# Optimization experiments

Measured on AMD Instinct MI355X. Metric: run time of the kernel, lower is better.

## Reference

```python
import jax, jax.numpy as jnp
import numpy as np

N = 50000      # nodes
E = 600000     # edges (avg degree 12)
F_IN = 64      # raw node features
HID = 128      # hidden_size
HEADS = 8
DH = HID // HEADS  # 16, per-head dim = out_channels
C = 10         # classes
L = 3          # num_gnn_layers


def setup_inputs() -> dict:
    key = jax.random.key(0)
    ks = jax.random.split(key, 12)
    g = lambda k, shape, fan: jax.random.normal(k, shape, jnp.float32) / np.float32(np.sqrt(fan))
    return {
        "x": jax.random.normal(ks[0], (N, F_IN), jnp.float32),
        "edge_index": jax.random.randint(ks[1], (2, E), 0, N, dtype=jnp.int32),
        "distance": jax.random.uniform(ks[2], (E, 1), jnp.float32),
        "Wq": g(ks[3], (L, HID, HID), HID), "bq": jnp.zeros((L, HID), jnp.float32),
        "Wk": g(ks[4], (L, HID, HID), HID), "bk": jnp.zeros((L, HID), jnp.float32),
        "Wv": g(ks[5], (L, HID, HID), HID), "bv": jnp.zeros((L, HID), jnp.float32),
        "We": g(ks[6], (L, 1, HID), 1),
        "Ws": g(ks[7], (L, HID, HID), HID), "bs": jnp.zeros((L, HID), jnp.float32),
        "ln_g": jnp.ones((L, HID), jnp.float32), "ln_b": jnp.zeros((L, HID), jnp.float32),
        "W_before": g(ks[8], (F_IN, HID), F_IN), "b_before": jnp.zeros((HID,), jnp.float32),
        "W_after": g(ks[9], (HID, C), HID), "b_after": jnp.zeros((C,), jnp.float32),
    }


def _layer_norm(h, gamma, beta):
    m = h.mean(-1, keepdims=True)
    v = ((h - m) ** 2).mean(-1, keepdims=True)
    return (h - m) * jax.lax.rsqrt(v + 1e-5) * gamma + beta


def _transformer_conv(h, src, dst, ea, Wq, bq, Wk, bk, Wv, bv, We, Ws, bs):
    # PyG TransformerConv (concat=True, beta=False, root_weight=True), eval mode (no dropout)
    q = (h @ Wq + bq).reshape(-1, HEADS, DH)   # [N,H,D]
    k = (h @ Wk + bk).reshape(-1, HEADS, DH)
    v = (h @ Wv + bv).reshape(-1, HEADS, DH)
    e = (ea @ We).reshape(-1, HEADS, DH)       # [E,H,D] edge embedding (no bias)
    ke = k[src] + e                            # gather keys along edges
    alpha = (q[dst] * ke).sum(-1) / np.float32(np.sqrt(DH))  # [E,H]
    # segment softmax over incoming edges per destination node
    amax = jax.ops.segment_max(alpha, dst, num_segments=N)
    amax = jnp.where(jnp.isfinite(amax), amax, 0.0)
    ex = jnp.exp(alpha - amax[dst])
    den = jax.ops.segment_sum(ex, dst, num_segments=N)
    a = ex / (den[dst] + 1e-16)                # [E,H]
    msg = (v[src] + e) * a[..., None]          # weighted values
    out = jax.ops.segment_sum(msg, dst, num_segments=N).reshape(-1, HEADS * DH)
    return out + h @ Ws + bs                   # root/skip connection


def reference(x, edge_index, distance, Wq, bq, Wk, bk, Wv, bv, We, Ws, bs,
              ln_g, ln_b, W_before, b_before, W_after, b_after):
    src, dst = edge_index[0], edge_index[1]
    h = jax.nn.relu(x @ W_before + b_before)   # fcnn_before
    for i in range(L):
        h = _transformer_conv(h, src, dst, distance,
                              Wq[i], bq[i], Wk[i], bk[i], Wv[i], bv[i],
                              We[i], Ws[i], bs[i])
        if i < L - 1:
            h = jax.nn.relu(_layer_norm(h, ln_g[i], ln_b[i]))
    # fcnn_after
    h = jax.nn.relu(_layer_norm(h, ln_g[L - 1], ln_b[L - 1]))
    h = h @ W_after + b_after
    return jax.nn.log_softmax(h, axis=1)
```

## Files before the change

kernel.cpp:

```cpp
#include <hip/hip_runtime.h>
#include <cstdint>
#include <cstddef>

#define NN 50000
#define NE 600000
#define FIN 64
#define HID 128
#define NCLS 10
#define NLAYER 3

#define QSCALE 0.36067376022224085f

typedef __bf16 bf16x8 __attribute__((ext_vector_type(8)));
typedef float f32x4 __attribute__((ext_vector_type(4)));
typedef float f32x2 __attribute__((ext_vector_type(2)));

__device__ __forceinline__ unsigned short f2bf(float f) {
    unsigned int u = __builtin_bit_cast(unsigned int, f);
    u += 0x7fffu + ((u >> 16) & 1u);
    return (unsigned short)(u >> 16);
}
__device__ __forceinline__ float bf2f(unsigned short s) {
    unsigned int u = ((unsigned int)s) << 16;
    return __builtin_bit_cast(float, u);
}
__device__ __forceinline__ float lo16f(unsigned int w) {
    return __builtin_bit_cast(float, w << 16);
}
__device__ __forceinline__ float hi16f(unsigned int w) {
    return __builtin_bit_cast(float, w & 0xffff0000u);
}

__global__ __launch_bounds__(256) void k_count(const int* __restrict__ edst,
                                               int* __restrict__ counts) {
    int e = blockIdx.x * 256 + threadIdx.x;
    if (e < NE) atomicAdd(&counts[edst[e]], 1);
}

__global__ __launch_bounds__(512) void k_scan1(const int* __restrict__ counts,
                                               int* __restrict__ row_ptr,
                                               int* __restrict__ partials, int n) {
    __shared__ int sm[512];
    int tid = threadIdx.x;
    int i = blockIdx.x * 512 + tid;
    int v = (i < n) ? counts[i] : 0;
    sm[tid] = v;
    __syncthreads();
    #pragma unroll
    for (int off = 1; off < 512; off <<= 1) {
        int t = (tid >= off) ? sm[tid - off] : 0;
        __syncthreads();
        sm[tid] += t;
        __syncthreads();
    }
    if (i < n) row_ptr[i] = sm[tid] - v;
    if (tid == 511) partials[blockIdx.x] = sm[511];
}

__global__ __launch_bounds__(128) void k_scan2(int* __restrict__ partials, int nb) {
    __shared__ int sm[128];
    int t = threadIdx.x;
    int v = (t < nb) ? partials[t] : 0;
    sm[t] = v;
    __syncthreads();
    #pragma unroll
    for (int off = 1; off < 128; off <<= 1) {
        int x = (t >= off) ? sm[t - off] : 0;
        __syncthreads();
        sm[t] += x;
        __syncthreads();
    }
    if (t < nb) partials[t] = sm[t] - v;
}

__global__ __launch_bounds__(512) void k_scan3(int* __restrict__ row_ptr,
                                               const int* __restrict__ partials, int n) {
    int i = blockIdx.x * 512 + threadIdx.x;
    if (i < n) row_ptr[i] += partials[blockIdx.x];
}

__global__ __launch_bounds__(256) void k_fill(const int* __restrict__ esrc,
                                              const int* __restrict__ edst,
                                              const float* __restrict__ dist,
                                              int* __restrict__ cursor,
                                              const int* __restrict__ row_ptr,
                                              int2* __restrict__ srcd) {
    int e = blockIdx.x * 256 + threadIdx.x;
    if (e < NE) {
        int d = edst[e];
        int pos = atomicAdd(&cursor[d], 1);
        srcd[row_ptr[d] + pos] = make_int2(esrc[e], __float_as_int(dist[e]));
    }
}

__global__ __launch_bounds__(256) void k_wprep(
    const float* __restrict__ Wq, const float* __restrict__ Wk,
    const float* __restrict__ Wv, const float* __restrict__ Ws,
    const float* __restrict__ Wbe, const float* __restrict__ Waf,
    unsigned short* __restrict__ Wt12,
    unsigned short* __restrict__ Wbt,
    float* __restrict__ Wat)
{
    int blk = blockIdx.x;
    int tid = threadIdx.x;
    if (blk < 768) {
        int m = blk >> 6;
        int l = m >> 2, which = m & 3;
        const float* src;
        if (which == 0) src = Wq; else if (which == 1) src = Wk;
        else if (which == 2) src = Wv; else src = Ws;
        src += (size_t)l * HID * HID;
        int idx = (blk & 63) * 256 + tid;
        int c = idx >> 7, k = idx & 127;
        Wt12[(size_t)m * 16384 + (size_t)c * 128 + k] = f2bf(src[(size_t)k * 128 + c]);
    } else if (blk < 800) {
        int idx = (blk - 768) * 256 + tid;
        int c = idx >> 6, k = idx & 63;
        Wbt[(size_t)c * 64 + k] = f2bf(Wbe[(size_t)k * 128 + c]);
    } else {
        int i = (blk - 800) * 256 + tid;
        if (i < 1280) {
            int c = i >> 7, f = i & 127;
            Wat[i] = Waf[f * 10 + c];
        }
    }
}

__global__ __launch_bounds__(512) void k_qkvs(
    const unsigned short* __restrict__ Ab, int nrows,
    const unsigned short* __restrict__ Wt,
    const float* __restrict__ bq, const float* __restrict__ bk,
    const float* __restrict__ bv, const float* __restrict__ bs,
    unsigned short* __restrict__ qb,
    unsigned char* __restrict__ kv8,
    unsigned short* __restrict__ hsb)
{
    const int tid = threadIdx.x;
    const int w = tid >> 6, lane = tid & 63;
    const int m = w >> 1, ch = w & 1;
    const float* bias = (m == 0) ? bq : (m == 1) ? bk : (m == 2) ? bv : bs;
    const unsigned short* Wm = Wt + (size_t)m * 16384;
    const int lc = lane & 15, lk = lane >> 4;

    bf16x8 b[4][4];
    float bb[4];
    #pragma unroll
    for (int ct = 0; ct < 4; ++ct) {
        int col = ch * 64 + ct * 16 + lc;
        bb[ct] = bias[col];
        #pragma unroll
        for (int kb = 0; kb < 4; ++kb)
            b[ct][kb] = *(const bf16x8*)(Wm + (size_t)col * 128 + kb * 32 + lk * 8);
    }

    const int r0 = blockIdx.x * 64;
    #pragma unroll
    for (int rt = 0; rt < 4; ++rt) {
        const int arow = r0 + rt * 16 + lc;
        bf16x8 z = {};
        bf16x8 a[4];
        #pragma unroll
        for (int kb = 0; kb < 4; ++kb)
            a[kb] = (arow < nrows) ? *(const bf16x8*)(Ab + (size_t)arow * 128 + kb * 32 + lk * 8) : z;
        #pragma unroll
        for (int ct = 0; ct < 4; ++ct) {
            f32x4 acc = {0.f, 0.f, 0.f, 0.f};
            #pragma unroll
            for (int kb = 0; kb < 4; ++kb)
                acc = __builtin_amdgcn_mfma_f32_16x16x32_bf16(a[kb], b[ct][kb], acc, 0, 0, 0);
            const int col = ch * 64 + ct * 16 + lc;
            #pragma unroll
            for (int i = 0; i < 4; ++i) {
                int r = r0 + rt * 16 + lk * 4 + i;
                if (r >= nrows) continue;
                float val = acc[i] + bb[ct];
                if (m == 0) {
                    qb[(size_t)r * 128 + col] = f2bf(val * QSCALE);
                } else if (m == 1) {
                    unsigned int pk = __builtin_amdgcn_cvt_pk_fp8_f32(val, val, 0, false);
                    kv8[(size_t)r * 256 + col] = (unsigned char)(pk & 0xff);
                } else if (m == 2) {
                    unsigned int pk = __builtin_amdgcn_cvt_pk_fp8_f32(val, val, 0, false);
                    kv8[(size_t)r * 256 + 128 + col] = (unsigned char)(pk & 0xff);
                } else {
                    hsb[(size_t)r * 128 + col] = f2bf(val);
                }
            }
        }
    }
}

__global__ __launch_bounds__(256) void k_gin(
    const float* __restrict__ x, int nrows,
    const unsigned short* __restrict__ Wt,
    const float* __restrict__ bias,
    unsigned short* __restrict__ hb)
{
    const int tid = threadIdx.x;
    const int w = tid >> 6, lane = tid & 63;
    const int row0 = blockIdx.x * 64 + w * 16;
    const int lc = lane & 15, lk = lane >> 4;
    const int arow = row0 + lc;
    const bool rv = arow < nrows;

    bf16x8 a[2];
    #pragma unroll
    for (int kb = 0; kb < 2; ++kb) {
        union { bf16x8 v; unsigned short u[8]; } t;
        #pragma unroll
        for (int q = 0; q < 2; ++q) {
            float4 f = rv ? *(const float4*)(x + (size_t)arow * 64 + kb * 32 + lk * 8 + q * 4)
                          : make_float4(0.f, 0.f, 0.f, 0.f);
            t.u[q * 4 + 0] = f2bf(f.x); t.u[q * 4 + 1] = f2bf(f.y);
            t.u[q * 4 + 2] = f2bf(f.z); t.u[q * 4 + 3] = f2bf(f.w);
        }
        a[kb] = t.v;
    }

    const int cbase = lk * 4;
    #pragma unroll
    for (int ct = 0; ct < 8; ++ct) {
        const int bcol = ct * 16 + lc;
        f32x4 acc = {0.f, 0.f, 0.f, 0.f};
        #pragma unroll
        for (int kb = 0; kb < 2; ++kb) {
            bf16x8 b = *(const bf16x8*)(Wt + (size_t)bcol * 64 + kb * 32 + lk * 8);
            acc = __builtin_amdgcn_mfma_f32_16x16x32_bf16(a[kb], b, acc, 0, 0, 0);
        }
        const float bv_ = bias[bcol];
        #pragma unroll
        for (int i = 0; i < 4; ++i) {
            int r = row0 + cbase + i;
            if (r >= nrows) continue;
            hb[(size_t)r * 128 + bcol] = f2bf(fmaxf(acc[i] + bv_, 0.f));
        }
    }
}

#define LOADB(bi, kw, vw, dd, vv) {                                       \
    int rel_ = (bi) * 8 + j;                                              \
    vv = rel_ < cnt;                                                      \
    if (vv) {                                                             \
        int2 e2_ = srcd[beg + rel_];                                      \
        dd = __int_as_float(e2_.y);                                       \
        const unsigned char* kr_ = kvb + (size_t)e2_.x * 256 + h * 16;    \
        *(uint4*)(kw) = *(const uint4*)(kr_);                             \
        *(uint4*)(vw) = *(const uint4*)(kr_ + 128);                       \
    } else {                                                              \
        dd = 0.f;                                                         \
        _Pragma("unroll")                                                 \
        for (int z_ = 0; z_ < 4; ++z_) { (kw)[z_] = 0u; (vw)[z_] = 0u; }  \
    } }

#define COMPB(kw, vw, dd, vv) {                                           \
    float p_ = 0.f;                                                       \
    _Pragma("unroll")                                                     \
    for (int w4 = 0; w4 < 4; ++w4) {                                      \
        f32x2 k01_ = __builtin_amdgcn_cvt_pk_f32_fp8((kw)[w4], false);    \
        f32x2 k23_ = __builtin_amdgcn_cvt_pk_f32_fp8((kw)[w4], true);     \
        p_ = fmaf(qf[4 * w4 + 0], k01_.x, p_);                            \
        p_ = fmaf(qf[4 * w4 + 1], k01_.y, p_);                            \
        p_ = fmaf(qf[4 * w4 + 2], k23_.x, p_);                            \
        p_ = fmaf(qf[4 * w4 + 3], k23_.y, p_);                            \
    }                                                                     \
    p_ = fmaf(dd, qwe, p_);                                               \
    float wgt_ = (vv) ? exp2f(p_) : 0.f;                                  \
    s += wgt_;                                                            \
    sd = fmaf(dd, wgt_, sd);                                              \
    _Pragma("unroll")                                                     \
    for (int w4 = 0; w4 < 4; ++w4) {                                      \
        f32x2 v01_ = __builtin_amdgcn_cvt_pk_f32_fp8((vw)[w4], false);    \
        f32x2 v23_ = __builtin_amdgcn_cvt_pk_f32_fp8((vw)[w4], true);     \
        vacc[4 * w4 + 0] = fmaf(v01_.x, wgt_, vacc[4 * w4 + 0]);          \
        vacc[4 * w4 + 1] = fmaf(v01_.y, wgt_, vacc[4 * w4 + 1]);          \
        vacc[4 * w4 + 2] = fmaf(v23_.x, wgt_, vacc[4 * w4 + 2]);          \
        vacc[4 * w4 + 3] = fmaf(v23_.y, wgt_, vacc[4 * w4 + 3]);          \
    } }

template <int LAST>
__global__ __launch_bounds__(256) void k_attn(
    const unsigned short* __restrict__ qb,
    const unsigned short* __restrict__ hsb,
    const unsigned char* __restrict__ kvb,
    const int2* __restrict__ srcd,
    const float* __restrict__ We,
    const int* __restrict__ row_ptr,
    const float* __restrict__ lng,
    const float* __restrict__ lnb,
    unsigned short* __restrict__ hb,
    const float* __restrict__ Wat,
    const float* __restrict__ ba,
    float* __restrict__ out, int nnodes)
{
    const int wid = threadIdx.x >> 6;
    const int lane = threadIdx.x & 63;
    const int n = blockIdx.x * 4 + wid;
    if (n >= nnodes) return;
    const int h = lane >> 3, j = lane & 7;
    const int c0 = lane * 2;

    unsigned int uq[8];
    *(uint4*)(uq)     = *(const uint4*)(qb + (size_t)n * 128 + h * 16);
    *(uint4*)(uq + 4) = *(const uint4*)(qb + (size_t)n * 128 + h * 16 + 8);
    float qf[16];
    #pragma unroll
    for (int d = 0; d < 8; ++d) {
        qf[2 * d]     = lo16f(uq[d]);
        qf[2 * d + 1] = hi16f(uq[d]);
    }
    float qwe = 0.f;
    #pragma unroll
    for (int d4 = 0; d4 < 4; ++d4) {
        float4 wv = *(const float4*)(We + h * 16 + d4 * 4);
        qwe = fmaf(qf[d4 * 4 + 0], wv.x, qwe);
        qwe = fmaf(qf[d4 * 4 + 1], wv.y, qwe);
        qwe = fmaf(qf[d4 * 4 + 2], wv.z, qwe);
        qwe = fmaf(qf[d4 * 4 + 3], wv.w, qwe);
    }

    const int beg = row_ptr[n];
    const int cnt = row_ptr[n + 1] - beg;
    float s = 0.f, sd = 0.f;
    float vacc[16];
    #pragma unroll
    for (int d = 0; d < 16; ++d) vacc[d] = 0.f;

    if (cnt > 0) {
        const int nbatch = (cnt + 7) >> 3;
        unsigned int kwA[4], vwA[4], kwB[4], vwB[4], kwC[4], vwC[4];
        float dA = 0.f, dB = 0.f, dC = 0.f;
        bool vA = false, vB = false, vC = false;
        LOADB(0, kwA, vwA, dA, vA);
        if (1 < nbatch) LOADB(1, kwB, vwB, dB, vB);
        int b = 0;
        while (true) {
            if (b + 2 < nbatch) LOADB(b + 2, kwC, vwC, dC, vC);
            COMPB(kwA, vwA, dA, vA);
            if (++b >= nbatch) break;
            if (b + 2 < nbatch) LOADB(b + 2, kwA, vwA, dA, vA);
            COMPB(kwB, vwB, dB, vB);
            if (++b >= nbatch) break;
            if (b + 2 < nbatch) LOADB(b + 2, kwB, vwB, dB, vB);
            COMPB(kwC, vwC, dC, vC);
            if (++b >= nbatch) break;
        }
    }

    #pragma unroll
    for (int msk = 1; msk < 8; msk <<= 1) {
        s  += __shfl_xor(s, msk);
        sd += __shfl_xor(sd, msk);
    }
    const bool b4 = (lane & 4) != 0;
    float c8[8];
    #pragma unroll
    for (int i = 0; i < 8; ++i) {
        float sendv = b4 ? vacc[i] : vacc[8 + i];
        float keep  = b4 ? vacc[8 + i] : vacc[i];
        c8[i] = keep + __shfl_xor(sendv, 4);
    }
    const bool b2 = (lane & 2) != 0;
    float c4[4];
    #pragma unroll
    for (int i = 0; i < 4; ++i) {
        float sendv = b2 ? c8[i] : c8[4 + i];
        float keep  = b2 ? c8[4 + i] : c8[i];
        c4[i] = keep + __shfl_xor(sendv, 2);
    }
    const bool b1 = (lane & 1) != 0;
    float c2[2];
    #pragma unroll
    for (int i = 0; i < 2; ++i) {
        float sendv = b1 ? c4[i] : c4[2 + i];
        float keep  = b1 ? c4[2 + i] : c4[i];
        c2[i] = keep + __shfl_xor(sendv, 1);
    }

    const float inv = 1.f / (s + 1e-16f);
    const float we0 = We[c0], we1 = We[c0 + 1];
    const ushort2 hu = *(const ushort2*)(hsb + (size_t)n * 128 + c0);
    float o0 = fmaf(fmaf(we0, sd, c2[0]), inv, bf2f(hu.x));
    float o1 = fmaf(fmaf(we1, sd, c2[1]), inv, bf2f(hu.y));

    float t = o0 + o1;
    #pragma unroll
    for (int off = 1; off < 64; off <<= 1) t += __shfl_xor(t, off);
    float mean = t * 0.0078125f;
    float d0 = o0 - mean, d1 = o1 - mean;
    float vv2 = d0 * d0 + d1 * d1;
    #pragma unroll
    for (int off = 1; off < 64; off <<= 1) vv2 += __shfl_xor(vv2, off);
    float rstd = rsqrtf(vv2 * 0.0078125f + 1e-5f);
    float y0 = fmaxf(d0 * rstd * lng[c0] + lnb[c0], 0.f);
    float y1 = fmaxf(d1 * rstd * lng[c0 + 1] + lnb[c0 + 1], 0.f);

    if (LAST) {
        float lg[NCLS];
        #pragma unroll
        for (int c = 0; c < NCLS; ++c) {
            float2 wv = *(const float2*)(Wat + c * 128 + c0);
            float p = fmaf(y0, wv.x, y1 * wv.y);
            #pragma unroll
            for (int msk = 1; msk < 64; msk <<= 1) p += __shfl_xor(p, msk);
            lg[c] = p + ba[c];
        }
        float mx = lg[0];
        #pragma unroll
        for (int c = 1; c < NCLS; ++c) mx = fmaxf(mx, lg[c]);
        float sum = 0.f;
        #pragma unroll
        for (int c = 0; c < NCLS; ++c) sum += __expf(lg[c] - mx);
        float lse = mx + __logf(sum);
        if (lane == 0) {
            #pragma unroll
            for (int c = 0; c < NCLS; ++c) out[(size_t)n * NCLS + c] = lg[c] - lse;
        }
    } else {
        ushort2 o;
        o.x = f2bf(y0);
        o.y = f2bf(y1);
        *(ushort2*)(hb + (size_t)n * 128 + c0) = o;
    }
}

extern "C" void kernel_launch(void* const* d_in, const int* in_sizes, int n_in,
                              void* d_out, int out_size, void* d_ws, size_t ws_size,
                              hipStream_t stream)
{
    const float* x    = (const float*)d_in[0];
    const int*   ei   = (const int*)d_in[1];
    const float* dist = (const float*)d_in[2];
    const float* Wq   = (const float*)d_in[3];
    const float* bq   = (const float*)d_in[4];
    const float* Wk   = (const float*)d_in[5];
    const float* bk   = (const float*)d_in[6];
    const float* Wv   = (const float*)d_in[7];
    const float* bv   = (const float*)d_in[8];
    const float* We   = (const float*)d_in[9];
    const float* Wsk  = (const float*)d_in[10];
    const float* bs   = (const float*)d_in[11];
    const float* lng  = (const float*)d_in[12];
    const float* lnb  = (const float*)d_in[13];
    const float* Wbe  = (const float*)d_in[14];
    const float* bbe  = (const float*)d_in[15];
    const float* Waf  = (const float*)d_in[16];
    const float* baf  = (const float*)d_in[17];
    float* out = (float*)d_out;
    const int* esrc = ei;
    const int* edst = ei + NE;

    char* ws = (char*)d_ws;
    size_t off = 0;
    unsigned short* qb  = (unsigned short*)(ws + off); off += 12800000;
    unsigned short* hsb = (unsigned short*)(ws + off); off += 12800000;
    unsigned char*  kv8 = (unsigned char*)(ws + off);  off += 12800000;
    unsigned short* hb  = (unsigned short*)(ws + off); off += 12800000;
    unsigned short* Wt12 = (unsigned short*)(ws + off); off += 393216;
    unsigned short* Wbt  = (unsigned short*)(ws + off); off += 16384;
    float* Wat = (float*)(ws + off);   off += 5120;
    int* counts   = (int*)(ws + off);  off += 200192;
    int* cursor   = (int*)(ws + off);  off += 200192;
    int* row_ptr  = (int*)(ws + off);  off += 200192;
    int* partials = (int*)(ws + off);  off += 512;
    int2* srcd    = (int2*)(ws + off); off += (size_t)NE * 8;

    hipMemsetAsync(counts, 0, (NN + 1) * sizeof(int), stream);
    hipMemsetAsync(cursor, 0, NN * sizeof(int), stream);
    k_count<<<(NE + 255) / 256, 256, 0, stream>>>(edst, counts);
    int nsb = (NN + 1 + 511) / 512;
    k_scan1<<<nsb, 512, 0, stream>>>(counts, row_ptr, partials, NN + 1);
    k_scan2<<<1, 128, 0, stream>>>(partials, nsb);
    k_scan3<<<nsb, 512, 0, stream>>>(row_ptr, partials, NN + 1);
    k_fill<<<(NE + 255) / 256, 256, 0, stream>>>(esrc, edst, dist, cursor, row_ptr, srcd);

    k_wprep<<<805, 256, 0, stream>>>(Wq, Wk, Wv, Wsk, Wbe, Waf, Wt12, Wbt, Wat);

    const int ngb = (NN + 63) / 64;

    k_gin<<<ngb, 256, 0, stream>>>(x, NN, Wbt, bbe, hb);

    for (int l = 0; l < NLAYER; ++l) {
        const unsigned short* wt = Wt12 + (size_t)l * 4 * 16384;
        k_qkvs<<<ngb, 512, 0, stream>>>(hb, NN, wt,
            bq + l * HID, bk + l * HID, bv + l * HID, bs + l * HID,
            qb, kv8, hsb);
        if (l < NLAYER - 1) {
            k_attn<0><<<(NN + 3) / 4, 256, 0, stream>>>(qb, hsb, kv8, srcd, We + l * HID,
                row_ptr, lng + l * HID, lnb + l * HID, hb, nullptr, nullptr, nullptr, NN);
        } else {
            k_attn<1><<<(NN + 3) / 4, 256, 0, stream>>>(qb, hsb, kv8, srcd, We + l * HID,
                row_ptr, lng + l * HID, lnb + l * HID, hb, Wat, baf, out, NN);
        }
    }
}
```

Measured before the change: 396.1 us.

## Process two nodes per wave in attention, vectorize GEMM stores, fuse prep kernels

```diff
diff --git a/kernel.cpp b/kernel.cpp
--- a/kernel.cpp
+++ b/kernel.cpp
@@ -31,75 +31,14 @@
     return __builtin_bit_cast(float, w & 0xffff0000u);
 }
 
-__global__ __launch_bounds__(256) void k_count(const int* __restrict__ edst,
-                                               int* __restrict__ counts) {
-    int e = blockIdx.x * 256 + threadIdx.x;
-    if (e < NE) atomicAdd(&counts[edst[e]], 1);
-}
-
-__global__ __launch_bounds__(512) void k_scan1(const int* __restrict__ counts,
-                                               int* __restrict__ row_ptr,
-                                               int* __restrict__ partials, int n) {
-    __shared__ int sm[512];
-    int tid = threadIdx.x;
-    int i = blockIdx.x * 512 + tid;
-    int v = (i < n) ? counts[i] : 0;
-    sm[tid] = v;
-    __syncthreads();
-    #pragma unroll
-    for (int off = 1; off < 512; off <<= 1) {
-        int t = (tid >= off) ? sm[tid - off] : 0;
-        __syncthreads();
-        sm[tid] += t;
-        __syncthreads();
-    }
-    if (i < n) row_ptr[i] = sm[tid] - v;
-    if (tid == 511) partials[blockIdx.x] = sm[511];
-}
-
-__global__ __launch_bounds__(128) void k_scan2(int* __restrict__ partials, int nb) {
-    __shared__ int sm[128];
-    int t = threadIdx.x;
-    int v = (t < nb) ? partials[t] : 0;
-    sm[t] = v;
-    __syncthreads();
-    #pragma unroll
-    for (int off = 1; off < 128; off <<= 1) {
-        int x = (t >= off) ? sm[t - off] : 0;
-        __syncthreads();
-        sm[t] += x;
-        __syncthreads();
-    }
-    if (t < nb) partials[t] = sm[t] - v;
-}
-
-__global__ __launch_bounds__(512) void k_scan3(int* __restrict__ row_ptr,
-                                               const int* __restrict__ partials, int n) {
-    int i = blockIdx.x * 512 + threadIdx.x;
-    if (i < n) row_ptr[i] += partials[blockIdx.x];
-}
-
-__global__ __launch_bounds__(256) void k_fill(const int* __restrict__ esrc,
-                                              const int* __restrict__ edst,
-                                              const float* __restrict__ dist,
-                                              int* __restrict__ cursor,
-                                              const int* __restrict__ row_ptr,
-                                              int2* __restrict__ srcd) {
-    int e = blockIdx.x * 256 + threadIdx.x;
-    if (e < NE) {
-        int d = edst[e];
-        int pos = atomicAdd(&cursor[d], 1);
-        srcd[row_ptr[d] + pos] = make_int2(esrc[e], __float_as_int(dist[e]));
-    }
-}
-
-__global__ __launch_bounds__(256) void k_wprep(
+__global__ __launch_bounds__(256) void k_prep(
     const float* __restrict__ Wq, const float* __restrict__ Wk,
     const float* __restrict__ Wv, const float* __restrict__ Ws,
     const float* __restrict__ Wbe, const float* __restrict__ Waf,
     unsigned short* __restrict__ Wt12,
     unsigned short* __restrict__ Wbt,
-    float* __restrict__ Wat)
+    float* __restrict__ Wat,
+    const int* __restrict__ edst, int* __restrict__ counts)
 {
     int blk = blockIdx.x;
     int tid = threadIdx.x;
@@ -117,12 +56,71 @@
         int idx = (blk - 768) * 256 + tid;
         int c = idx >> 6, k = idx & 63;
         Wbt[(size_t)c * 64 + k] = f2bf(Wbe[(size_t)k * 128 + c]);
-    } else {
+    } else if (blk < 805) {
         int i = (blk - 800) * 256 + tid;
         if (i < 1280) {
             int c = i >> 7, f = i & 127;
             Wat[i] = Waf[f * 10 + c];
         }
+    } else {
+        int e = (blk - 805) * 256 + tid;
+        if (e < NE) atomicAdd(&counts[edst[e]], 1);
+    }
+}
+
+__global__ __launch_bounds__(512) void k_scan1(const int* __restrict__ counts,
+                                               int* __restrict__ row_ptr,
+                                               int* __restrict__ partials, int n) {
+    __shared__ int sm[512];
+    int tid = threadIdx.x;
+    int i = blockIdx.x * 512 + tid;
+    int v = (i < n) ? counts[i] : 0;
+    sm[tid] = v;
+    __syncthreads();
+    #pragma unroll
+    for (int off = 1; off < 512; off <<= 1) {
+        int t = (tid >= off) ? sm[tid - off] : 0;
+        __syncthreads();
+        sm[tid] += t;
+        __syncthreads();
+    }
+    if (i < n) row_ptr[i] = sm[tid] - v;
+    if (tid == 511) partials[blockIdx.x] = sm[511];
+}
+
+__global__ __launch_bounds__(128) void k_scan2(int* __restrict__ partials, int nb) {
+    __shared__ int sm[128];
+    int t = threadIdx.x;
+    int v = (t < nb) ? partials[t] : 0;
+    sm[t] = v;
+    __syncthreads();
+    #pragma unroll
+    for (int off = 1; off < 128; off <<= 1) {
+        int x = (t >= off) ? sm[t - off] : 0;
+        __syncthreads();
+        sm[t] += x;
+        __syncthreads();
+    }
+    if (t < nb) partials[t] = sm[t] - v;
+}
+
+__global__ __launch_bounds__(512) void k_scan3(int* __restrict__ row_ptr,
+                                               const int* __restrict__ partials, int n) {
+    int i = blockIdx.x * 512 + threadIdx.x;
+    if (i < n) row_ptr[i] += partials[blockIdx.x];
+}
+
+__global__ __launch_bounds__(256) void k_fill(const int* __restrict__ esrc,
+                                              const int* __restrict__ edst,
+                                              const float* __restrict__ dist,
+                                              int* __restrict__ cursor,
+                                              const int* __restrict__ row_ptr,
+                                              int2* __restrict__ srcd) {
+    int e = blockIdx.x * 256 + threadIdx.x;
+    if (e < NE) {
+        int d = edst[e];
+        int pos = atomicAdd(&cursor[d], 1);
+        srcd[row_ptr[d] + pos] = make_int2(esrc[e], __float_as_int(dist[e]));
     }
 }
 
@@ -142,48 +140,50 @@
     const unsigned short* Wm = Wt + (size_t)m * 16384;
     const int lc = lane & 15, lk = lane >> 4;
 
-    bf16x8 b[4][4];
-    float bb[4];
+    bf16x8 bw[4][4];
+    float4 bb[4];
     #pragma unroll
     for (int ct = 0; ct < 4; ++ct) {
         int col = ch * 64 + ct * 16 + lc;
-        bb[ct] = bias[col];
+        bb[ct] = *(const float4*)(bias + ch * 64 + ct * 16 + lk * 4);
         #pragma unroll
         for (int kb = 0; kb < 4; ++kb)
-            b[ct][kb] = *(const bf16x8*)(Wm + (size_t)col * 128 + kb * 32 + lk * 8);
+            bw[ct][kb] = *(const bf16x8*)(Wm + (size_t)col * 128 + kb * 32 + lk * 8);
     }
 
     const int r0 = blockIdx.x * 64;
     #pragma unroll
     for (int rt = 0; rt < 4; ++rt) {
         const int arow = r0 + rt * 16 + lc;
+        const bool rv = arow < nrows;
         bf16x8 z = {};
         bf16x8 a[4];
         #pragma unroll
         for (int kb = 0; kb < 4; ++kb)
-            a[kb] = (arow < nrows) ? *(const bf16x8*)(Ab + (size_t)arow * 128 + kb * 32 + lk * 8) : z;
+            a[kb] = rv ? *(const bf16x8*)(Ab + (size_t)arow * 128 + kb * 32 + lk * 8) : z;
         #pragma unroll
         for (int ct = 0; ct < 4; ++ct) {
             f32x4 acc = {0.f, 0.f, 0.f, 0.f};
             #pragma unroll
             for (int kb = 0; kb < 4; ++kb)
-                acc = __builtin_amdgcn_mfma_f32_16x16x32_bf16(a[kb], b[ct][kb], acc, 0, 0, 0);
-            const int col = ch * 64 + ct * 16 + lc;
-            #pragma unroll
-            for (int i = 0; i < 4; ++i) {
-                int r = r0 + rt * 16 + lk * 4 + i;
-                if (r >= nrows) continue;
-                float val = acc[i] + bb[ct];
+                acc = __builtin_amdgcn_mfma_f32_16x16x32_bf16(bw[ct][kb], a[kb], acc, 0, 0, 0);
+            if (rv) {
+                const int colb = ch * 64 + ct * 16 + lk * 4;
+                float v0 = acc[0] + bb[ct].x, v1 = acc[1] + bb[ct].y;
+                float v2 = acc[2] + bb[ct].z, v3 = acc[3] + bb[ct].w;
                 if (m == 0) {
-                    qb[(size_t)r * 128 + col] = f2bf(val * QSCALE);
-                } else if (m == 1) {
-                    unsigned int pk = __builtin_amdgcn_cvt_pk_fp8_f32(val, val, 0, false);
-                    kv8[(size_t)r * 256 + col] = (unsigned char)(pk & 0xff);
-                } else if (m == 2) {
-                    unsigned int pk = __builtin_amdgcn_cvt_pk_fp8_f32(val, val, 0, false);
-                    kv8[(size_t)r * 256 + 128 + col] = (unsigned char)(pk & 0xff);
+                    ushort4 o;
+                    o.x = f2bf(v0 * QSCALE); o.y = f2bf(v1 * QSCALE);
+                    o.z = f2bf(v2 * QSCALE); o.w = f2bf(v3 * QSCALE);
+                    *(ushort4*)(qb + (size_t)arow * 128 + colb) = o;
+                } else if (m == 1 || m == 2) {
+                    unsigned int pk = __builtin_amdgcn_cvt_pk_fp8_f32(v0, v1, 0, false);
+                    pk = __builtin_amdgcn_cvt_pk_fp8_f32(v2, v3, pk, true);
+                    *(unsigned int*)(kv8 + (size_t)arow * 256 + (m == 2 ? 128 : 0) + colb) = pk;
                 } else {
-                    hsb[(size_t)r * 128 + col] = f2bf(val);
+                    ushort4 o;
+                    o.x = f2bf(v0); o.y = f2bf(v1); o.z = f2bf(v2); o.w = f2bf(v3);
+                    *(ushort4*)(hsb + (size_t)arow * 128 + colb) = o;
                 }
             }
         }
@@ -198,9 +198,8 @@
 {
     const int tid = threadIdx.x;
     const int w = tid >> 6, lane = tid & 63;
-    const int row0 = blockIdx.x * 64 + w * 16;
     const int lc = lane & 15, lk = lane >> 4;
-    const int arow = row0 + lc;
+    const int arow = blockIdx.x * 64 + w * 16 + lc;
     const bool rv = arow < nrows;
 
     bf16x8 a[2];
@@ -217,42 +216,49 @@
         a[kb] = t.v;
     }
 
-    const int cbase = lk * 4;
     #pragma unroll
     for (int ct = 0; ct < 8; ++ct) {
-        const int bcol = ct * 16 + lc;
         f32x4 acc = {0.f, 0.f, 0.f, 0.f};
         #pragma unroll
         for (int kb = 0; kb < 2; ++kb) {
-            bf16x8 b = *(const bf16x8*)(Wt + (size_t)bcol * 64 + kb * 32 + lk * 8);
-            acc = __builtin_amdgcn_mfma_f32_16x16x32_bf16(a[kb], b, acc, 0, 0, 0);
-        }
-        const float bv_ = bias[bcol];
-        #pragma unroll
-        for (int i = 0; i < 4; ++i) {
-            int r = row0 + cbase + i;
-            if (r >= nrows) continue;
-            hb[(size_t)r * 128 + bcol] = f2bf(fmaxf(acc[i] + bv_, 0.f));
-        }
-    }
-}
-
-#define LOADB(bi, kw, vw, dd, vv) {                                       \
-    int rel_ = (bi) * 8 + j;                                              \
-    vv = rel_ < cnt;                                                      \
+            bf16x8 bwf = *(const bf16x8*)(Wt + (size_t)(ct * 16 + lc) * 64 + kb * 32 + lk * 8);
+            acc = __builtin_amdgcn_mfma_f32_16x16x32_bf16(bwf, a[kb], acc, 0, 0, 0);
+        }
+        if (rv) {
+            float4 bv_ = *(const float4*)(bias + ct * 16 + lk * 4);
+            ushort4 o;
+            o.x = f2bf(fmaxf(acc[0] + bv_.x, 0.f));
+            o.y = f2bf(fmaxf(acc[1] + bv_.y, 0.f));
+            o.z = f2bf(fmaxf(acc[2] + bv_.z, 0.f));
+            o.w = f2bf(fmaxf(acc[3] + bv_.w, 0.f));
+            *(ushort4*)(hb + (size_t)arow * 128 + ct * 16 + lk * 4) = o;
+        }
+    }
+}
+
+#define EFETCH(relbase, t, cntN, kw, vw, dd, vv) {                        \
+    int rel_ = (relbase) + (t) * 8 + j;                                   \
+    vv = (t) * 8 + j < (cntN);                                            \
+    int r6_ = rel_ & 63;                                                  \
+    int ax_ = __shfl(w0.x, r6_), ay_ = __shfl(w0.y, r6_);                 \
+    int bx_ = __shfl(w1.x, r6_), by_ = __shfl(w1.y, r6_);                 \
+    int sx_ = rel_ < 64 ? ax_ : bx_;                                      \
+    int sy_ = rel_ < 64 ? ay_ : by_;                                      \
+    if (vv && rel_ >= 128) {                                              \
+        int2 e2_ = srcd[beg0 + rel_];                                     \
+        sx_ = e2_.x; sy_ = e2_.y;                                         \
+    }                                                                     \
+    dd = vv ? __int_as_float(sy_) : 0.f;                                  \
     if (vv) {                                                             \
-        int2 e2_ = srcd[beg + rel_];                                      \
-        dd = __int_as_float(e2_.y);                                       \
-        const unsigned char* kr_ = kvb + (size_t)e2_.x * 256 + h * 16;    \
+        const unsigned char* kr_ = kvb + (size_t)sx_ * 256 + h * 16;      \
         *(uint4*)(kw) = *(const uint4*)(kr_);                             \
         *(uint4*)(vw) = *(const uint4*)(kr_ + 128);                       \
     } else {                                                              \
-        dd = 0.f;                                                         \
         _Pragma("unroll")                                                 \
         for (int z_ = 0; z_ < 4; ++z_) { (kw)[z_] = 0u; (vw)[z_] = 0u; }  \
     } }
 
-#define COMPB(kw, vw, dd, vv) {                                           \
+#define COMPB(kw, vw, dd, vv, qf, qwe, s, sd, vacc) {                     \
     float p_ = 0.f;                                                       \
     _Pragma("unroll")                                                     \
     for (int w4 = 0; w4 < 4; ++w4) {                                      \
@@ -278,7 +284,7 @@
     } }
 
 template <int LAST>
-__global__ __launch_bounds__(256) void k_attn(
+__global__ __launch_bounds__(256, 4) void k_attn(
     const unsigned short* __restrict__ qb,
     const unsigned short* __restrict__ hsb,
     const unsigned char* __restrict__ kvb,
@@ -294,132 +300,182 @@
 {
     const int wid = threadIdx.x >> 6;
     const int lane = threadIdx.x & 63;
-    const int n = blockIdx.x * 4 + wid;
-    if (n >= nnodes) return;
+    const int n0 = (blockIdx.x * 4 + wid) * 2;
+    if (n0 >= nnodes) return;
+    const int n1 = n0 + 1;
     const int h = lane >> 3, j = lane & 7;
     const int c0 = lane * 2;
 
-    unsigned int uq[8];
-    *(uint4*)(uq)     = *(const uint4*)(qb + (size_t)n * 128 + h * 16);
-    *(uint4*)(uq + 4) = *(const uint4*)(qb + (size_t)n * 128 + h * 16 + 8);
-    float qf[16];
+    int rpv = 0;
+    if (lane < 3) rpv = row_ptr[n0 + lane];
+    const int beg0 = __shfl(rpv, 0);
+    const int beg1 = __shfl(rpv, 1);
+    const int end1 = __shfl(rpv, 2);
+    const int cnt0 = beg1 - beg0;
+    const int cnt1 = end1 - beg1;
+    const int T = end1 - beg0;
+
+    int2 w0 = make_int2(0, 0), w1 = make_int2(0, 0);
+    if (lane < T) w0 = srcd[beg0 + lane];
+    if (64 + lane < T) w1 = srcd[beg0 + 64 + lane];
+
+    unsigned int uq0[8], uq1[8];
+    *(uint4*)(uq0)     = *(const uint4*)(qb + (size_t)n0 * 128 + h * 16);
+    *(uint4*)(uq0 + 4) = *(const uint4*)(qb + (size_t)n0 * 128 + h * 16 + 8);
+    *(uint4*)(uq1)     = *(const uint4*)(qb + (size_t)n1 * 128 + h * 16);
+    *(uint4*)(uq1 + 4) = *(const uint4*)(qb + (size_t)n1 * 128 + h * 16 + 8);
+    const ushort2 hu0 = *(const ushort2*)(hsb + (size_t)n0 * 128 + c0);
+    const ushort2 hu1 = *(const ushort2*)(hsb + (size_t)n1 * 128 + c0);
+
+    float qf0[16], qf1[16];
     #pragma unroll
     for (int d = 0; d < 8; ++d) {
-        qf[2 * d]     = lo16f(uq[d]);
-        qf[2 * d + 1] = hi16f(uq[d]);
-    }
-    float qwe = 0.f;
+        qf0[2 * d] = lo16f(uq0[d]); qf0[2 * d + 1] = hi16f(uq0[d]);
+        qf1[2 * d] = lo16f(uq1[d]); qf1[2 * d + 1] = hi16f(uq1[d]);
+    }
+    float qwe0 = 0.f, qwe1 = 0.f;
     #pragma unroll
     for (int d4 = 0; d4 < 4; ++d4) {
         float4 wv = *(const float4*)(We + h * 16 + d4 * 4);
-        qwe = fmaf(qf[d4 * 4 + 0], wv.x, qwe);
-        qwe = fmaf(qf[d4 * 4 + 1], wv.y, qwe);
-        qwe = fmaf(qf[d4 * 4 + 2], wv.z, qwe);
-        qwe = fmaf(qf[d4 * 4 + 3], wv.w, qwe);
-    }
-
-    const int beg = row_ptr[n];
-    const int cnt = row_ptr[n + 1] - beg;
-    float s = 0.f, sd = 0.f;
-    float vacc[16];
-    #pragma unroll
-    for (int d = 0; d < 16; ++d) vacc[d] = 0.f;
-
-    if (cnt > 0) {
-        const int nbatch = (cnt + 7) >> 3;
-        unsigned int kwA[4], vwA[4], kwB[4], vwB[4], kwC[4], vwC[4];
-        float dA = 0.f, dB = 0.f, dC = 0.f;
-        bool vA = false, vB = false, vC = false;
-        LOADB(0, kwA, vwA, dA, vA);
-        if (1 < nbatch) LOADB(1, kwB, vwB, dB, vB);
-        int b = 0;
-        while (true) {
-            if (b + 2 < nbatch) LOADB(b + 2, kwC, vwC, dC, vC);
-            COMPB(kwA, vwA, dA, vA);
-            if (++b >= nbatch) break;
-            if (b + 2 < nbatch) LOADB(b + 2, kwA, vwA, dA, vA);
-            COMPB(kwB, vwB, dB, vB);
-            if (++b >= nbatch) break;
-            if (b + 2 < nbatch) LOADB(b + 2, kwB, vwB, dB, vB);
-            COMPB(kwC, vwC, dC, vC);
-            if (++b >= nbatch) break;
+        qwe0 = fmaf(qf0[d4 * 4 + 0], wv.x, qwe0); qwe1 = fmaf(qf1[d4 * 4 + 0], wv.x, qwe1);
+        qwe0 = fmaf(qf0[d4 * 4 + 1], wv.y, qwe0); qwe1 = fmaf(qf1[d4 * 4 + 1], wv.y, qwe1);
+        qwe0 = fmaf(qf0[d4 * 4 + 2], wv.z, qwe0); qwe1 = fmaf(qf1[d4 * 4 + 2], wv.z, qwe1);
+        qwe0 = fmaf(qf0[d4 * 4 + 3], wv.w, qwe0); qwe1 = fmaf(qf1[d4 * 4 + 3], wv.w, qwe1);
+    }
+
+    float s0 = 0.f, sd0 = 0.f, s1 = 0.f, sd1 = 0.f;
+    float vacc0[16], vacc1[16];
+    #pragma unroll
+    for (int d = 0; d < 16; ++d) { vacc0[d] = 0.f; vacc1[d] = 0.f; }
+
+    {
+        const int nb0 = (cnt0 + 7) >> 3, nb1 = (cnt1 + 7) >> 3;
+        unsigned int kA[4], vA[4], kB[4], vB[4], kC[4], vC[4], kD[4], vD[4];
+        float dA, dB, dC, dD;
+        bool eA, eB, eC, eD;
+        EFETCH(0,    0, cnt0, kA, vA, dA, eA);
+        EFETCH(cnt0, 0, cnt1, kB, vB, dB, eB);
+        EFETCH(0,    1, cnt0, kC, vC, dC, eC);
+        EFETCH(cnt0, 1, cnt1, kD, vD, dD, eD);
+        COMPB(kA, vA, dA, eA, qf0, qwe0, s0, sd0, vacc0);
+        COMPB(kB, vB, dB, eB, qf1, qwe1, s1, sd1, vacc1);
+        COMPB(kC, vC, dC, eC, qf0, qwe0, s0, sd0, vacc0);
+        COMPB(kD, vD, dD, eD, qf1, qwe1, s1, sd1, vacc1);
+        const int tmax = nb0 > nb1 ? nb0 : nb1;
+        for (int t = 2; t < tmax; ++t) {
+            EFETCH(0,    t, cnt0, kA, vA, dA, eA);
+            EFETCH(cnt0, t, cnt1, kB, vB, dB, eB);
+            COMPB(kA, vA, dA, eA, qf0, qwe0, s0, sd0, vacc0);
+            COMPB(kB, vB, dB, eB, qf1, qwe1, s1, sd1, vacc1);
         }
     }
 
     #pragma unroll
     for (int msk = 1; msk < 8; msk <<= 1) {
-        s  += __shfl_xor(s, msk);
-        sd += __shfl_xor(sd, msk);
+        s0  += __shfl_xor(s0, msk);  sd0 += __shfl_xor(sd0, msk);
+        s1  += __shfl_xor(s1, msk);  sd1 += __shfl_xor(sd1, msk);
     }
     const bool b4 = (lane & 4) != 0;
-    float c8[8];
+    float c8a[8], c8b[8];
     #pragma unroll
     for (int i = 0; i < 8; ++i) {
-        float sendv = b4 ? vacc[i] : vacc[8 + i];
-        float keep  = b4 ? vacc[8 + i] : vacc[i];
-        c8[i] = keep + __shfl_xor(sendv, 4);
+        float sa = b4 ? vacc0[i] : vacc0[8 + i];
+        float ka = b4 ? vacc0[8 + i] : vacc0[i];
+        c8a[i] = ka + __shfl_xor(sa, 4);
+        float sb = b4 ? vacc1[i] : vacc1[8 + i];
+        float kb = b4 ? vacc1[8 + i] : vacc1[i];
+        c8b[i] = kb + __shfl_xor(sb, 4);
     }
     const bool b2 = (lane & 2) != 0;
-    float c4[4];
+    float c4a[4], c4b[4];
     #pragma unroll
     for (int i = 0; i < 4; ++i) {
-        float sendv = b2 ? c8[i] : c8[4 + i];
-        float keep  = b2 ? c8[4 + i] : c8[i];
-        c4[i] = keep + __shfl_xor(sendv, 2);
+        float sa = b2 ? c8a[i] : c8a[4 + i];
+        float ka = b2 ? c8a[4 + i] : c8a[i];
+        c4a[i] = ka + __shfl_xor(sa, 2);
+        float sb = b2 ? c8b[i] : c8b[4 + i];
+        float kb = b2 ? c8b[4 + i] : c8b[i];
+        c4b[i] = kb + __shfl_xor(sb, 2);
     }
     const bool b1 = (lane & 1) != 0;
-    float c2[2];
+    float c2a[2], c2b[2];
     #pragma unroll
     for (int i = 0; i < 2; ++i) {
-        float sendv = b1 ? c4[i] : c4[2 + i];
-        float keep  = b1 ? c4[2 + i] : c4[i];
-        c2[i] = keep + __shfl_xor(sendv, 1);
-    }
-
-    const float inv = 1.f / (s + 1e-16f);
-    const float we0 = We[c0], we1 = We[c0 + 1];
-    const ushort2 hu = *(const ushort2*)(hsb + (size_t)n * 128 + c0);
-    float o0 = fmaf(fmaf(we0, sd, c2[0]), inv, bf2f(hu.x));
-    float o1 = fmaf(fmaf(we1, sd, c2[1]), inv, bf2f(hu.y));
-
-    float t = o0 + o1;
-    #pragma unroll
-    for (int off = 1; off < 64; off <<= 1) t += __shfl_xor(t, off);
-    float mean = t * 0.0078125f;
-    float d0 = o0 - mean, d1 = o1 - mean;
-    float vv2 = d0 * d0 + d1 * d1;
-    #pragma unroll
-    for (int off = 1; off < 64; off <<= 1) vv2 += __shfl_xor(vv2, off);
-    float rstd = rsqrtf(vv2 * 0.0078125f + 1e-5f);
-    float y0 = fmaxf(d0 * rstd * lng[c0] + lnb[c0], 0.f);
-    float y1 = fmaxf(d1 * rstd * lng[c0 + 1] + lnb[c0 + 1], 0.f);
+        float sa = b1 ? c4a[i] : c4a[2 + i];
+        float ka = b1 ? c4a[2 + i] : c4a[i];
+        c2a[i] = ka + __shfl_xor(sa, 1);
+        float sb = b1 ? c4b[i] : c4b[2 + i];
+        float kb = b1 ? c4b[2 + i] : c4b[i];
+        c2b[i] = kb + __shfl_xor(sb, 1);
+    }
+
+    const float inv0 = 1.f / (s0 + 1e-16f);
+    const float inv1 = 1.f / (s1 + 1e-16f);
+    const float2 wev = *(const float2*)(We + c0);
+    float o00 = fmaf(fmaf(wev.x, sd0, c2a[0]), inv0, bf2f(hu0.x));
+    float o01 = fmaf(fmaf(wev.y, sd0, c2a[1]), inv0, bf2f(hu0.y));
+    float o10 = fmaf(fmaf(wev.x, sd1, c2b[0]), inv1, bf2f(hu1.x));
+    float o11 = fmaf(fmaf(wev.y, sd1, c2b[1]), inv1, bf2f(hu1.y));
+
+    float t0 = o00 + o01, t1 = o10 + o11;
+    #pragma unroll
+    for (int off = 1; off < 64; off <<= 1) {
+        t0 += __shfl_xor(t0, off);
+        t1 += __shfl_xor(t1, off);
+    }
+    const float mean0 = t0 * 0.0078125f, mean1 = t1 * 0.0078125f;
+    float d00 = o00 - mean0, d01 = o01 - mean0;
+    float d10 = o10 - mean1, d11 = o11 - mean1;
+    float v0 = d00 * d00 + d01 * d01, v1 = d10 * d10 + d11 * d11;
+    #pragma unroll
+    for (int off = 1; off < 64; off <<= 1) {
+        v0 += __shfl_xor(v0, off);
+        v1 += __shfl_xor(v1, off);
+    }
+    const float rstd0 = rsqrtf(v0 * 0.0078125f + 1e-5f);
+    const float rstd1 = rsqrtf(v1 * 0.0078125f + 1e-5f);
+    const float2 g2 = *(const float2*)(lng + c0);
+    const float2 be2 = *(const float2*)(lnb + c0);
+    float y00 = fmaxf(fmaf(d00 * rstd0, g2.x, be2.x), 0.f);
+    float y01 = fmaxf(fmaf(d01 * rstd0, g2.y, be2.y), 0.f);
+    float y10 = fmaxf(fmaf(d10 * rstd1, g2.x, be2.x), 0.f);
+    float y11 = fmaxf(fmaf(d11 * rstd1, g2.y, be2.y), 0.f);
 
     if (LAST) {
-        float lg[NCLS];
+        float lg0[NCLS], lg1[NCLS];
         #pragma unroll
         for (int c = 0; c < NCLS; ++c) {
             float2 wv = *(const float2*)(Wat + c * 128 + c0);
-            float p = fmaf(y0, wv.x, y1 * wv.y);
+            float p0 = fmaf(y00, wv.x, y01 * wv.y);
+            float p1 = fmaf(y10, wv.x, y11 * wv.y);
             #pragma unroll
-            for (int msk = 1; msk < 64; msk <<= 1) p += __shfl_xor(p, msk);
-            lg[c] = p + ba[c];
-        }
-        float mx = lg[0];
-        #pragma unroll
-        for (int c = 1; c < NCLS; ++c) mx = fmaxf(mx, lg[c]);
-        float sum = 0.f;
-        #pragma unroll
-        for (int c = 0; c < NCLS; ++c) sum += __expf(lg[c] - mx);
-        float lse = mx + __logf(sum);
+            for (int msk = 1; msk < 64; msk <<= 1) {
+                p0 += __shfl_xor(p0, msk);
+                p1 += __shfl_xor(p1, msk);
+            }
+            lg0[c] = p0 + ba[c];
+            lg1[c] = p1 + ba[c];
+        }
+        float mx0 = lg0[0], mx1 = lg1[0];
+        #pragma unroll
+        for (int c = 1; c < NCLS; ++c) { mx0 = fmaxf(mx0, lg0[c]); mx1 = fmaxf(mx1, lg1[c]); }
+        float su0 = 0.f, su1 = 0.f;
+        #pragma unroll
+        for (int c = 0; c < NCLS; ++c) { su0 += __expf(lg0[c] - mx0); su1 += __expf(lg1[c] - mx1); }
+        float lse0 = mx0 + __logf(su0), lse1 = mx1 + __logf(su1);
         if (lane == 0) {
             #pragma unroll
-            for (int c = 0; c < NCLS; ++c) out[(size_t)n * NCLS + c] = lg[c] - lse;
+            for (int c = 0; c < NCLS; ++c) {
+                out[(size_t)n0 * NCLS + c] = lg0[c] - lse0;
+                out[(size_t)n1 * NCLS + c] = lg1[c] - lse1;
+            }
         }
     } else {
-        ushort2 o;
-        o.x = f2bf(y0);
-        o.y = f2bf(y1);
-        *(ushort2*)(hb + (size_t)n * 128 + c0) = o;
+        ushort2 oa, ob;
+        oa.x = f2bf(y00); oa.y = f2bf(y01);
+        ob.x = f2bf(y10); ob.y = f2bf(y11);
+        *(ushort2*)(hb + (size_t)n0 * 128 + c0) = oa;
+        *(ushort2*)(hb + (size_t)n1 * 128 + c0) = ob;
     }
 }
 
@@ -464,17 +520,15 @@
     int* partials = (int*)(ws + off);  off += 512;
     int2* srcd    = (int2*)(ws + off); off += (size_t)NE * 8;
 
-    hipMemsetAsync(counts, 0, (NN + 1) * sizeof(int), stream);
-    hipMemsetAsync(cursor, 0, NN * sizeof(int), stream);
-    k_count<<<(NE + 255) / 256, 256, 0, stream>>>(edst, counts);
+    hipMemsetAsync(counts, 0, 2 * 200192, stream);
+    k_prep<<<805 + (NE + 255) / 256, 256, 0, stream>>>(
+        Wq, Wk, Wv, Wsk, Wbe, Waf, Wt12, Wbt, Wat, edst, counts);
     int nsb = (NN + 1 + 511) / 512;
     k_scan1<<<nsb, 512, 0, stream>>>(counts, row_ptr, partials, NN + 1);
     k_scan2<<<1, 128, 0, stream>>>(partials, nsb);
     k_scan3<<<nsb, 512, 0, stream>>>(row_ptr, partials, NN + 1);
     k_fill<<<(NE + 255) / 256, 256, 0, stream>>>(esrc, edst, dist, cursor, row_ptr, srcd);
 
-    k_wprep<<<805, 256, 0, stream>>>(Wq, Wk, Wv, Wsk, Wbe, Waf, Wt12, Wbt, Wat);
-
     const int ngb = (NN + 63) / 64;
 
     k_gin<<<ngb, 256, 0, stream>>>(x, NN, Wbt, bbe, hb);
@@ -484,11 +538,12 @@
         k_qkvs<<<ngb, 512, 0, stream>>>(hb, NN, wt,
             bq + l * HID, bk + l * HID, bv + l * HID, bs + l * HID,
             qb, kv8, hsb);
+        const int nab = (NN / 2 + 3) / 4;
         if (l < NLAYER - 1) {
-            k_attn<0><<<(NN + 3) / 4, 256, 0, stream>>>(qb, hsb, kv8, srcd, We + l * HID,
+            k_attn<0><<<nab, 256, 0, stream>>>(qb, hsb, kv8, srcd, We + l * HID,
                 row_ptr, lng + l * HID, lnb + l * HID, hb, nullptr, nullptr, nullptr, NN);
         } else {
-            k_attn<1><<<(NN + 3) / 4, 256, 0, stream>>>(qb, hsb, kv8, srcd, We + l * HID,
+            k_attn<1><<<nab, 256, 0, stream>>>(qb, hsb, kv8, srcd, We + l * HID,
                 row_ptr, lng + l * HID, lnb + l * HID, hb, Wat, baf, out, NN);
         }
     }
```

Result: faster. 345.8 us (-12.7%).
